# Optimization experiments

Measured on AMD Instinct MI355X. Metric: run time of the kernel, lower is better.

The kernel has to match this reference:

```python
import jax, jax.numpy as jnp
import numpy as np

PI = np.pi
WIN = (8, 8)
N = WIN[0] * WIN[1]          # 64 tokens per window
NUM_HEADS = 8
DIM = 256
HEAD_DIM = DIM // NUM_HEADS  # 32
P = 4                        # Fourier series order (hardcoded in module)
W_RES = 64                   # input_resolution[1]
SCALE = HEAD_DIM ** -0.5
B_ = 1024                    # num_windows * batch


def _azimuth():
    # relative_coords[:, :, 1] from the torch module: relative column offsets
    ch = np.arange(WIN[0])
    cw = np.arange(WIN[1])
    gh, gw = np.meshgrid(ch, cw, indexing='ij')
    cf = np.stack([gh.ravel(), gw.ravel()])          # (2, N)
    rel = cf[:, :, None] - cf[:, None, :]            # (2, N, N)
    return jnp.asarray(rel[1], dtype=jnp.float32)    # (N, N)


def setup_inputs() -> dict:
    key = jax.random.key(0)
    ks = jax.random.split(key, 12)
    std = 0.02
    return {
        'x': jax.random.normal(ks[0], (B_, N, DIM), dtype=jnp.float32),
        'D': jax.random.uniform(ks[1], (B_, N), dtype=jnp.float32),
        'a_p': std * jax.random.normal(ks[2], (P + 1, NUM_HEADS), dtype=jnp.float32),
        'b_p': std * jax.random.normal(ks[3], (P, NUM_HEADS), dtype=jnp.float32),
        'a_r': std * jax.random.normal(ks[4], (P + 1, NUM_HEADS), dtype=jnp.float32),
        'b_r': std * jax.random.normal(ks[5], (P, NUM_HEADS), dtype=jnp.float32),
        'qkv_w': std * jax.random.normal(ks[6], (3 * DIM, DIM), dtype=jnp.float32),
        'qkv_b': jnp.zeros((3 * DIM,), dtype=jnp.float32),
        'proj_w': std * jax.random.normal(ks[7], (DIM, DIM), dtype=jnp.float32),
        'proj_b': jnp.zeros((DIM,), dtype=jnp.float32),
    }


def reference(x, D, a_p, b_p, a_r, b_r, qkv_w, qkv_b, proj_w, proj_b):
    B, n, C = x.shape

    # ---- azimuth Fourier bias: A_phi, shape (H, N, N) ----
    az = _azimuth() * (2.0 * PI / W_RES)                       # (N, N)
    ii = jnp.arange(1, P + 1, dtype=x.dtype)[:, None, None]    # (P, 1, 1)
    cosP = jnp.cos(ii * az)                                    # (P, N, N)
    sinP = jnp.sin(ii * az)
    A_phi = (jnp.einsum('ph,pij->hij', a_p[1:], cosP)
             + jnp.einsum('ph,pij->hij', b_p, sinP)) / P + a_p[0][:, None, None]

    # ---- radius Fourier bias: A_r, shape (B, N, N, H); rad[b,i,j] = D[b,j] - D[b,i] ----
    rad = D[:, None, :] - D[:, :, None]                        # (B, N, N)
    r_max = 2.0                                                # module overwrites r_max = 2
    A_r = jnp.zeros(rad.shape + (NUM_HEADS,), dtype=x.dtype)
    for i in range(1, P + 1):
        arg = rad * (2.0 * PI * i / r_max)
        A_r = A_r + jnp.cos(arg)[..., None] * a_r[i] + jnp.sin(arg)[..., None] * b_r[i - 1]
    A_r = A_r / P + a_r[0]                                     # (B, N, N, H)

    # ---- attention ----
    qkv = (x @ qkv_w.T + qkv_b).reshape(B, n, 3, NUM_HEADS, HEAD_DIM)
    qkv = qkv.transpose(2, 0, 3, 1, 4)                         # (3, B, H, N, hd)
    q, k, v = qkv[0], qkv[1], qkv[2]
    attn = jnp.einsum('bhid,bhjd->bhij', q * SCALE, k)
    attn = attn + A_phi[None] + A_r.transpose(0, 3, 1, 2)
    attn = jax.nn.softmax(attn, axis=-1)
    out = jnp.einsum('bhij,bhjd->bhid', attn, v)
    out = out.transpose(0, 2, 1, 3).reshape(B, n, C)
    return out @ proj_w.T + proj_b
```

## Files before the change

kernel.cpp:

```cpp
#include <hip/hip_runtime.h>
#include <hip/hip_bf16.h>


using short8  = __attribute__((ext_vector_type(8))) short;
using floatx4 = __attribute__((ext_vector_type(4))) float;

#define PI_F    3.14159265358979323846f
#define SCALE_F 0.17677669529663687f

__global__ void prep_kernel(const float* __restrict__ qw,
                            const float* __restrict__ pw,
                            __hip_bfloat16* __restrict__ dst) {
  int g = blockIdx.x * 256 + threadIdx.x;
  const float4* src;
  __hip_bfloat16* d;
  if (g < 49152) { src = (const float4*)qw + g; d = dst + g * 4; }
  else { int g2 = g - 49152; src = (const float4*)pw + g2; d = dst + 196608 + g2 * 4; }
  float4 v = *src;
  d[0] = __float2bfloat16(v.x);
  d[1] = __float2bfloat16(v.y);
  d[2] = __float2bfloat16(v.z);
  d[3] = __float2bfloat16(v.w);
}

__device__ __forceinline__ void fourier_feats(float dv, int col, float* f) {
  float s1, c1; __sincosf(PI_F * dv, &s1, &c1);
  float c2 = c1*c1 - s1*s1, s2 = 2.f*s1*c1;
  float c3 = c2*c1 - s2*s1, s3 = s2*c1 + c2*s1;
  float c4 = c2*c2 - s2*s2, s4 = 2.f*s2*c2;
  float sa1, ca1; __sincosf((2.f * PI_F / 64.f) * (float)col, &sa1, &ca1);
  float ca2 = ca1*ca1 - sa1*sa1, sa2 = 2.f*sa1*ca1;
  float ca3 = ca2*ca1 - sa2*sa1, sa3 = sa2*ca1 + ca2*sa1;
  float ca4 = ca2*ca2 - sa2*sa2, sa4 = 2.f*sa2*ca2;
  f[0]=c1;  f[1]=c2;  f[2]=c3;  f[3]=c4;
  f[4]=s1;  f[5]=s2;  f[6]=s3;  f[7]=s4;
  f[8]=ca1; f[9]=ca2; f[10]=ca3; f[11]=ca4;
  f[12]=sa1; f[13]=sa2; f[14]=sa3; f[15]=sa4;
}

__global__ __launch_bounds__(512, 2) void fused_kernel(
    const float* __restrict__ x, const float* __restrict__ D,
    const float* __restrict__ a_p, const float* __restrict__ b_p,
    const float* __restrict__ a_r, const float* __restrict__ b_r,
    const __hip_bfloat16* __restrict__ wq, const float* __restrict__ qkv_b,
    const __hip_bfloat16* __restrict__ pwb, const float* __restrict__ pb,
    float* __restrict__ out)
{
  constexpr int LDX = 264, LDQ = 264, LDK = 264, LDQf = 40, LDKm = 136,
                LDVt = 72, LDP = 72, LDO = 264;
  __shared__ __align__(16) __hip_bfloat16 sScr[64 * 264];
  __shared__ __align__(16) __hip_bfloat16 sQ  [64 * 264];
  __shared__ __align__(16) __hip_bfloat16 sK  [64 * 264];
  __shared__ __align__(16) __hip_bfloat16 sQf [64 * 40];
  __shared__ __align__(16) __hip_bfloat16 sKm [64 * 136];
  __shared__ __align__(16) __hip_bfloat16 sVt [256 * 72];

  const int tid = threadIdx.x;
  const int lane = tid & 63, w = tid >> 6;
  const int laneN = lane & 15, laneQ = lane >> 4;
  const int b = blockIdx.x;
  const floatx4 fzero = {0.f, 0.f, 0.f, 0.f};
  const short8 zero8 = {0, 0, 0, 0, 0, 0, 0, 0};

  const float4* xg = (const float4*)(x + (size_t)b * 16384);
  #pragma unroll
  for (int it = 0; it < 8; ++it) {
    int g = tid + it * 512;
    float4 v = xg[g];
    int t = g >> 6, c = (g & 63) * 4;
    __hip_bfloat16* p = &sScr[t * LDX + c];
    p[0] = __float2bfloat16(v.x); p[1] = __float2bfloat16(v.y);
    p[2] = __float2bfloat16(v.z); p[3] = __float2bfloat16(v.w);
  }
  if (tid < 64) {
    float f[16];
    fourier_feats(D[b * 64 + tid], tid & 7, f);
    #pragma unroll
    for (int i = 0; i < 16; ++i) sQf[tid * LDQf + i] = __float2bfloat16(f[i]);
    #pragma unroll
    for (int i = 16; i < 32; ++i) sQf[tid * LDQf + i] = __float2bfloat16(0.f);
  }
  __syncthreads();

  {
    int t = tid >> 3, hh = tid & 7;
    float f[16];
    fourier_feats(D[b * 64 + t], t & 7, f);
    #pragma unroll
    for (int p = 0; p < 4; ++p) {
      float ar = a_r[(p + 1) * 8 + hh], br = b_r[p * 8 + hh];
      float ap = a_p[(p + 1) * 8 + hh], bp = b_p[p * 8 + hh];
      float cr = f[p], sr = f[4 + p], ca = f[8 + p], sa = f[12 + p];
      sKm[t * LDKm + hh * 16 +  0 + p] = __float2bfloat16((ar * cr + br * sr) * 0.25f);
      sKm[t * LDKm + hh * 16 +  4 + p] = __float2bfloat16((ar * sr - br * cr) * 0.25f);
      sKm[t * LDKm + hh * 16 +  8 + p] = __float2bfloat16((ap * ca - bp * sa) * 0.25f);
      sKm[t * LDKm + hh * 16 + 12 + p] = __float2bfloat16((ap * sa + bp * ca) * 0.25f);
    }
  }

  short8 afq[4][8];
  #pragma unroll
  for (int mt = 0; mt < 4; ++mt)
    #pragma unroll
    for (int kk = 0; kk < 8; ++kk)
      afq[mt][kk] = *(const short8*)&sScr[(mt * 16 + laneN) * LDX + kk * 32 + laneQ * 8];

  #pragma unroll
  for (int ni = 0; ni < 6; ++ni) {
    int col0 = (w * 6 + ni) * 16;
    float bias = qkv_b[col0 + laneN];
    short8 bq[8];
    #pragma unroll
    for (int kk = 0; kk < 8; ++kk)
      bq[kk] = *(const short8*)&wq[(size_t)(col0 + laneN) * 256 + kk * 32 + laneQ * 8];
    floatx4 acc[4] = {fzero, fzero, fzero, fzero};
    #pragma unroll
    for (int kk = 0; kk < 8; ++kk)
      #pragma unroll
      for (int mt = 0; mt < 4; ++mt)
        acc[mt] = __builtin_amdgcn_mfma_f32_16x16x32_bf16(afq[mt][kk], bq[kk], acc[mt], 0, 0, 0);
    if (col0 < 256) {
      #pragma unroll
      for (int mt = 0; mt < 4; ++mt)
        #pragma unroll
        for (int r = 0; r < 4; ++r)
          sQ[(mt * 16 + laneQ * 4 + r) * LDQ + col0 + laneN] =
              __float2bfloat16((acc[mt][r] + bias) * SCALE_F);
    } else if (col0 < 512) {
      #pragma unroll
      for (int mt = 0; mt < 4; ++mt)
        #pragma unroll
        for (int r = 0; r < 4; ++r)
          sK[(mt * 16 + laneQ * 4 + r) * LDK + (col0 - 256) + laneN] =
              __float2bfloat16(acc[mt][r] + bias);
    } else {
      int vd = col0 - 512 + laneN;
      #pragma unroll
      for (int mt = 0; mt < 4; ++mt)
        #pragma unroll
        for (int r = 0; r < 4; ++r)
          sVt[vd * LDVt + (mt * 16 + laneQ * 4 + r)] = __float2bfloat16(acc[mt][r] + bias);
    }
  }
  __syncthreads();

  const int h = w;
  short8 qf0[4], qf1[4], kf0[4], kf1[4];
  #pragma unroll
  for (int mt = 0; mt < 4; ++mt) {
    qf0[mt] = *(const short8*)&sQ[(mt * 16 + laneN) * LDQ + h * 32 + laneQ * 8];
    qf1[mt] = *(const short8*)&sQf[(mt * 16 + laneN) * LDQf + laneQ * 8];
  }
  #pragma unroll
  for (int nt = 0; nt < 4; ++nt) {
    kf0[nt] = *(const short8*)&sK[(nt * 16 + laneN) * LDK + h * 32 + laneQ * 8];
    short8 km = *(const short8*)&sKm[(nt * 16 + laneN) * LDKm + h * 16 + (laneQ & 1) * 8];
    kf1[nt] = (laneQ < 2) ? km : zero8;
  }
  floatx4 s[4][4];
  #pragma unroll
  for (int mt = 0; mt < 4; ++mt)
    #pragma unroll
    for (int nt = 0; nt < 4; ++nt) {
      s[mt][nt] = __builtin_amdgcn_mfma_f32_16x16x32_bf16(qf0[mt], kf0[nt], fzero, 0, 0, 0);
      s[mt][nt] = __builtin_amdgcn_mfma_f32_16x16x32_bf16(qf1[mt], kf1[nt], s[mt][nt], 0, 0, 0);
    }

  short8 vb[2][2];
  #pragma unroll
  for (int ont = 0; ont < 2; ++ont)
    #pragma unroll
    for (int kk = 0; kk < 2; ++kk)
      vb[ont][kk] = *(const short8*)&sVt[(h * 32 + ont * 16 + laneN) * LDVt + kk * 32 + laneQ * 8];

  floatx4 oacc[4][2];
  __hip_bfloat16* Pw = &sScr[w * 16 * LDP];
  #pragma unroll
  for (int mt = 0; mt < 4; ++mt) {
    #pragma unroll
    for (int r = 0; r < 4; ++r) {
      float mx = fmaxf(fmaxf(s[mt][0][r], s[mt][1][r]), fmaxf(s[mt][2][r], s[mt][3][r]));
      mx = fmaxf(mx, __shfl_xor(mx, 1));
      mx = fmaxf(mx, __shfl_xor(mx, 2));
      mx = fmaxf(mx, __shfl_xor(mx, 4));
      mx = fmaxf(mx, __shfl_xor(mx, 8));
      float e0 = __expf(s[mt][0][r] - mx), e1 = __expf(s[mt][1][r] - mx);
      float e2 = __expf(s[mt][2][r] - mx), e3 = __expf(s[mt][3][r] - mx);
      float sum = e0 + e1 + e2 + e3;
      sum += __shfl_xor(sum, 1);
      sum += __shfl_xor(sum, 2);
      sum += __shfl_xor(sum, 4);
      sum += __shfl_xor(sum, 8);
      float inv = __builtin_amdgcn_rcpf(sum);
      int pr = laneQ * 4 + r;
      Pw[pr * LDP +  0 + laneN] = __float2bfloat16(e0 * inv);
      Pw[pr * LDP + 16 + laneN] = __float2bfloat16(e1 * inv);
      Pw[pr * LDP + 32 + laneN] = __float2bfloat16(e2 * inv);
      Pw[pr * LDP + 48 + laneN] = __float2bfloat16(e3 * inv);
    }
    short8 pf0 = *(const short8*)&Pw[laneN * LDP + laneQ * 8];
    short8 pf1 = *(const short8*)&Pw[laneN * LDP + 32 + laneQ * 8];
    #pragma unroll
    for (int ont = 0; ont < 2; ++ont) {
      oacc[mt][ont] = __builtin_amdgcn_mfma_f32_16x16x32_bf16(pf0, vb[ont][0], fzero, 0, 0, 0);
      oacc[mt][ont] = __builtin_amdgcn_mfma_f32_16x16x32_bf16(pf1, vb[ont][1], oacc[mt][ont], 0, 0, 0);
    }
  }
  __syncthreads();

  #pragma unroll
  for (int mt = 0; mt < 4; ++mt)
    #pragma unroll
    for (int ont = 0; ont < 2; ++ont)
      #pragma unroll
      for (int r = 0; r < 4; ++r)
        sScr[(mt * 16 + laneQ * 4 + r) * LDO + h * 32 + ont * 16 + laneN] =
            __float2bfloat16(oacc[mt][ont][r]);
  __syncthreads();

  const int col0 = w * 32;
  floatx4 pacc[4][2];
  #pragma unroll
  for (int mt = 0; mt < 4; ++mt) { pacc[mt][0] = fzero; pacc[mt][1] = fzero; }
  #pragma unroll
  for (int kk = 0; kk < 8; ++kk) {
    short8 pa[4], pbf[2];
    #pragma unroll
    for (int mt = 0; mt < 4; ++mt)
      pa[mt] = *(const short8*)&sScr[(mt * 16 + laneN) * LDO + kk * 32 + laneQ * 8];
    #pragma unroll
    for (int n2 = 0; n2 < 2; ++n2)
      pbf[n2] = *(const short8*)&pwb[(size_t)(col0 + n2 * 16 + laneN) * 256 + kk * 32 + laneQ * 8];
    #pragma unroll
    for (int mt = 0; mt < 4; ++mt)
      #pragma unroll
      for (int n2 = 0; n2 < 2; ++n2)
        pacc[mt][n2] = __builtin_amdgcn_mfma_f32_16x16x32_bf16(pa[mt], pbf[n2], pacc[mt][n2], 0, 0, 0);
  }
  float bias0 = pb[col0 + laneN], bias1 = pb[col0 + 16 + laneN];
  float* og = out + (size_t)b * 16384;
  #pragma unroll
  for (int mt = 0; mt < 4; ++mt)
    #pragma unroll
    for (int n2 = 0; n2 < 2; ++n2)
      #pragma unroll
      for (int r = 0; r < 4; ++r)
        og[(mt * 16 + laneQ * 4 + r) * 256 + col0 + n2 * 16 + laneN] =
            pacc[mt][n2][r] + (n2 ? bias1 : bias0);
}

extern "C" void kernel_launch(void* const* d_in, const int* in_sizes, int n_in,
                              void* d_out, int out_size, void* d_ws, size_t ws_size,
                              hipStream_t stream) {
  const float* x      = (const float*)d_in[0];
  const float* D      = (const float*)d_in[1];
  const float* a_p    = (const float*)d_in[2];
  const float* b_p    = (const float*)d_in[3];
  const float* a_r    = (const float*)d_in[4];
  const float* b_r    = (const float*)d_in[5];
  const float* qkv_w  = (const float*)d_in[6];
  const float* qkv_b  = (const float*)d_in[7];
  const float* proj_w = (const float*)d_in[8];
  const float* proj_b = (const float*)d_in[9];

  __hip_bfloat16* wq  = (__hip_bfloat16*)d_ws;
  __hip_bfloat16* pwb = wq + 196608;
  float* out = (float*)d_out;

  prep_kernel<<<256, 256, 0, stream>>>(qkv_w, proj_w, wq);
  fused_kernel<<<1024, 512, 0, stream>>>(x, D, a_p, b_p, a_r, b_r, wq, qkv_b,
                                         pwb, proj_b, out);
}
```

Measured before the change: 211.0 us.

## Double block to 1024 threads and split work across 16 waves with vectorized LDS stores

Launches 16 waves per window instead of 8. Each wave computes a 16-column slice of Q, K and V, half a head's query rows in attention, and a 16-column slice of the projection. MFMA operands are swapped so that results come out transposed and can be written as packed 4- or 8-element vector stores to LDS and as float4 global stores, instead of scalar bf16 and fp32 stores. The goal is more latency hiding per window and fewer LDS and global store instructions, at the cost of more per-wave K/V fragment loads and higher register pressure under launch bounds of 1024 threads with 4 blocks.

```diff
diff --git a/kernel.cpp b/kernel.cpp
--- a/kernel.cpp
+++ b/kernel.cpp
@@ -3,10 +3,16 @@
 
 
 using short8  = __attribute__((ext_vector_type(8))) short;
+using short4v = __attribute__((ext_vector_type(4))) short;
 using floatx4 = __attribute__((ext_vector_type(4))) float;
 
 #define PI_F    3.14159265358979323846f
 #define SCALE_F 0.17677669529663687f
+
+__device__ __forceinline__ short bfs(float x) {
+  __hip_bfloat16 h = __float2bfloat16(x);
+  return __builtin_bit_cast(short, h);
+}
 
 __global__ void prep_kernel(const float* __restrict__ qw,
                             const float* __restrict__ pw,
@@ -38,7 +44,7 @@
   f[12]=sa1; f[13]=sa2; f[14]=sa3; f[15]=sa4;
 }
 
-__global__ __launch_bounds__(512, 2) void fused_kernel(
+__global__ __launch_bounds__(1024, 4) void fused_kernel(
     const float* __restrict__ x, const float* __restrict__ D,
     const float* __restrict__ a_p, const float* __restrict__ b_p,
     const float* __restrict__ a_r, const float* __restrict__ b_r,
@@ -47,8 +53,8 @@
     float* __restrict__ out)
 {
   constexpr int LDX = 264, LDQ = 264, LDK = 264, LDQf = 40, LDKm = 136,
-                LDVt = 72, LDP = 72, LDO = 264;
-  __shared__ __align__(16) __hip_bfloat16 sScr[64 * 264];
+                LDVt = 72, LDP = 68, LDO = 264;
+  __shared__ __align__(16) __hip_bfloat16 sScr[17408];
   __shared__ __align__(16) __hip_bfloat16 sQ  [64 * 264];
   __shared__ __align__(16) __hip_bfloat16 sK  [64 * 264];
   __shared__ __align__(16) __hip_bfloat16 sQf [64 * 40];
@@ -64,108 +70,96 @@
 
   const float4* xg = (const float4*)(x + (size_t)b * 16384);
   #pragma unroll
-  for (int it = 0; it < 8; ++it) {
-    int g = tid + it * 512;
+  for (int it = 0; it < 4; ++it) {
+    int g = tid + it * 1024;
     float4 v = xg[g];
     int t = g >> 6, c = (g & 63) * 4;
-    __hip_bfloat16* p = &sScr[t * LDX + c];
-    p[0] = __float2bfloat16(v.x); p[1] = __float2bfloat16(v.y);
-    p[2] = __float2bfloat16(v.z); p[3] = __float2bfloat16(v.w);
+    short4v pk = { bfs(v.x), bfs(v.y), bfs(v.z), bfs(v.w) };
+    *(short4v*)&sScr[t * LDX + c] = pk;
   }
   if (tid < 64) {
     float f[16];
     fourier_feats(D[b * 64 + tid], tid & 7, f);
-    #pragma unroll
-    for (int i = 0; i < 16; ++i) sQf[tid * LDQf + i] = __float2bfloat16(f[i]);
-    #pragma unroll
-    for (int i = 16; i < 32; ++i) sQf[tid * LDQf + i] = __float2bfloat16(0.f);
-  }
-  __syncthreads();
-
-  {
+    short8 q0, q1;
+    #pragma unroll
+    for (int i = 0; i < 8; ++i) { q0[i] = bfs(f[i]); q1[i] = bfs(f[8 + i]); }
+    *(short8*)&sQf[tid * LDQf +  0] = q0;
+    *(short8*)&sQf[tid * LDQf +  8] = q1;
+    *(short8*)&sQf[tid * LDQf + 16] = zero8;
+    *(short8*)&sQf[tid * LDQf + 24] = zero8;
+  }
+  if (tid < 512) {
     int t = tid >> 3, hh = tid & 7;
     float f[16];
     fourier_feats(D[b * 64 + t], t & 7, f);
+    short8 v0, v1;
     #pragma unroll
     for (int p = 0; p < 4; ++p) {
       float ar = a_r[(p + 1) * 8 + hh], br = b_r[p * 8 + hh];
       float ap = a_p[(p + 1) * 8 + hh], bp = b_p[p * 8 + hh];
       float cr = f[p], sr = f[4 + p], ca = f[8 + p], sa = f[12 + p];
-      sKm[t * LDKm + hh * 16 +  0 + p] = __float2bfloat16((ar * cr + br * sr) * 0.25f);
-      sKm[t * LDKm + hh * 16 +  4 + p] = __float2bfloat16((ar * sr - br * cr) * 0.25f);
-      sKm[t * LDKm + hh * 16 +  8 + p] = __float2bfloat16((ap * ca - bp * sa) * 0.25f);
-      sKm[t * LDKm + hh * 16 + 12 + p] = __float2bfloat16((ap * sa + bp * ca) * 0.25f);
-    }
-  }
-
-  short8 afq[4][8];
-  #pragma unroll
-  for (int mt = 0; mt < 4; ++mt)
-    #pragma unroll
-    for (int kk = 0; kk < 8; ++kk)
-      afq[mt][kk] = *(const short8*)&sScr[(mt * 16 + laneN) * LDX + kk * 32 + laneQ * 8];
-
-  #pragma unroll
-  for (int ni = 0; ni < 6; ++ni) {
-    int col0 = (w * 6 + ni) * 16;
-    float bias = qkv_b[col0 + laneN];
-    short8 bq[8];
-    #pragma unroll
-    for (int kk = 0; kk < 8; ++kk)
-      bq[kk] = *(const short8*)&wq[(size_t)(col0 + laneN) * 256 + kk * 32 + laneQ * 8];
-    floatx4 acc[4] = {fzero, fzero, fzero, fzero};
-    #pragma unroll
-    for (int kk = 0; kk < 8; ++kk)
+      v0[p]     = bfs((ar * cr + br * sr) * 0.25f);
+      v0[4 + p] = bfs((ar * sr - br * cr) * 0.25f);
+      v1[p]     = bfs((ap * ca - bp * sa) * 0.25f);
+      v1[4 + p] = bfs((ap * sa + bp * ca) * 0.25f);
+    }
+    *(short8*)&sKm[t * LDKm + hh * 16 + 0] = v0;
+    *(short8*)&sKm[t * LDKm + hh * 16 + 8] = v1;
+  }
+  __syncthreads();
+
+  {
+    const __hip_bfloat16* w0 = wq + (size_t)(      w * 16 + laneN) * 256;
+    const __hip_bfloat16* w1 = wq + (size_t)(256 + w * 16 + laneN) * 256;
+    const __hip_bfloat16* w2 = wq + (size_t)(512 + w * 16 + laneN) * 256;
+    floatx4 accQ[4], accK[4], accV[4];
+    #pragma unroll
+    for (int mt = 0; mt < 4; ++mt) { accQ[mt] = fzero; accK[mt] = fzero; accV[mt] = fzero; }
+    #pragma unroll
+    for (int kk = 0; kk < 8; ++kk) {
+      short8 a4[4];
       #pragma unroll
       for (int mt = 0; mt < 4; ++mt)
-        acc[mt] = __builtin_amdgcn_mfma_f32_16x16x32_bf16(afq[mt][kk], bq[kk], acc[mt], 0, 0, 0);
-    if (col0 < 256) {
-      #pragma unroll
-      for (int mt = 0; mt < 4; ++mt)
-        #pragma unroll
-        for (int r = 0; r < 4; ++r)
-          sQ[(mt * 16 + laneQ * 4 + r) * LDQ + col0 + laneN] =
-              __float2bfloat16((acc[mt][r] + bias) * SCALE_F);
-    } else if (col0 < 512) {
-      #pragma unroll
-      for (int mt = 0; mt < 4; ++mt)
-        #pragma unroll
-        for (int r = 0; r < 4; ++r)
-          sK[(mt * 16 + laneQ * 4 + r) * LDK + (col0 - 256) + laneN] =
-              __float2bfloat16(acc[mt][r] + bias);
-    } else {
-      int vd = col0 - 512 + laneN;
-      #pragma unroll
-      for (int mt = 0; mt < 4; ++mt)
-        #pragma unroll
-        for (int r = 0; r < 4; ++r)
-          sVt[vd * LDVt + (mt * 16 + laneQ * 4 + r)] = __float2bfloat16(acc[mt][r] + bias);
-    }
-  }
-  __syncthreads();
-
-  const int h = w;
-  short8 qf0[4], qf1[4], kf0[4], kf1[4];
-  #pragma unroll
-  for (int mt = 0; mt < 4; ++mt) {
-    qf0[mt] = *(const short8*)&sQ[(mt * 16 + laneN) * LDQ + h * 32 + laneQ * 8];
-    qf1[mt] = *(const short8*)&sQf[(mt * 16 + laneN) * LDQf + laneQ * 8];
-  }
+        a4[mt] = *(const short8*)&sScr[(mt * 16 + laneN) * LDX + kk * 32 + laneQ * 8];
+      short8 b0 = *(const short8*)&w0[kk * 32 + laneQ * 8];
+      short8 b1 = *(const short8*)&w1[kk * 32 + laneQ * 8];
+      short8 b2 = *(const short8*)&w2[kk * 32 + laneQ * 8];
+      #pragma unroll
+      for (int mt = 0; mt < 4; ++mt) {
+        accQ[mt] = __builtin_amdgcn_mfma_f32_16x16x32_bf16(b0, a4[mt], accQ[mt], 0, 0, 0);
+        accK[mt] = __builtin_amdgcn_mfma_f32_16x16x32_bf16(b1, a4[mt], accK[mt], 0, 0, 0);
+        accV[mt] = __builtin_amdgcn_mfma_f32_16x16x32_bf16(a4[mt], b2, accV[mt], 0, 0, 0);
+      }
+    }
+    float4 bq4 = *(const float4*)&qkv_b[      w * 16 + laneQ * 4];
+    float4 bk4 = *(const float4*)&qkv_b[256 + w * 16 + laneQ * 4];
+    float bv   = qkv_b[512 + w * 16 + laneN];
+    float bqa[4] = {bq4.x, bq4.y, bq4.z, bq4.w};
+    float bka[4] = {bk4.x, bk4.y, bk4.z, bk4.w};
+    #pragma unroll
+    for (int mt = 0; mt < 4; ++mt) {
+      short4v pq, pk, pv;
+      #pragma unroll
+      for (int r = 0; r < 4; ++r) {
+        pq[r] = bfs((accQ[mt][r] + bqa[r]) * SCALE_F);
+        pk[r] = bfs(accK[mt][r] + bka[r]);
+        pv[r] = bfs(accV[mt][r] + bv);
+      }
+      *(short4v*)&sQ [(mt * 16 + laneN) * LDQ + w * 16 + laneQ * 4] = pq;
+      *(short4v*)&sK [(mt * 16 + laneN) * LDK + w * 16 + laneQ * 4] = pk;
+      *(short4v*)&sVt[(w * 16 + laneN) * LDVt + mt * 16 + laneQ * 4] = pv;
+    }
+  }
+  __syncthreads();
+
+  const int h = w >> 1, gm0 = (w & 1) * 2;
+  short8 kf0[4], kf1[4];
   #pragma unroll
   for (int nt = 0; nt < 4; ++nt) {
     kf0[nt] = *(const short8*)&sK[(nt * 16 + laneN) * LDK + h * 32 + laneQ * 8];
     short8 km = *(const short8*)&sKm[(nt * 16 + laneN) * LDKm + h * 16 + (laneQ & 1) * 8];
     kf1[nt] = (laneQ < 2) ? km : zero8;
   }
-  floatx4 s[4][4];
-  #pragma unroll
-  for (int mt = 0; mt < 4; ++mt)
-    #pragma unroll
-    for (int nt = 0; nt < 4; ++nt) {
-      s[mt][nt] = __builtin_amdgcn_mfma_f32_16x16x32_bf16(qf0[mt], kf0[nt], fzero, 0, 0, 0);
-      s[mt][nt] = __builtin_amdgcn_mfma_f32_16x16x32_bf16(qf1[mt], kf1[nt], s[mt][nt], 0, 0, 0);
-    }
-
   short8 vb[2][2];
   #pragma unroll
   for (int ont = 0; ont < 2; ++ont)
@@ -173,19 +167,28 @@
     for (int kk = 0; kk < 2; ++kk)
       vb[ont][kk] = *(const short8*)&sVt[(h * 32 + ont * 16 + laneN) * LDVt + kk * 32 + laneQ * 8];
 
-  floatx4 oacc[4][2];
+  floatx4 oacc[2][2];
   __hip_bfloat16* Pw = &sScr[w * 16 * LDP];
   #pragma unroll
-  for (int mt = 0; mt < 4; ++mt) {
+  for (int m = 0; m < 2; ++m) {
+    const int gm = gm0 + m;
+    short8 q0 = *(const short8*)&sQ [(gm * 16 + laneN) * LDQ + h * 32 + laneQ * 8];
+    short8 q1 = *(const short8*)&sQf[(gm * 16 + laneN) * LDQf + laneQ * 8];
+    floatx4 s[4];
+    #pragma unroll
+    for (int nt = 0; nt < 4; ++nt) {
+      s[nt] = __builtin_amdgcn_mfma_f32_16x16x32_bf16(q0, kf0[nt], fzero, 0, 0, 0);
+      s[nt] = __builtin_amdgcn_mfma_f32_16x16x32_bf16(q1, kf1[nt], s[nt], 0, 0, 0);
+    }
     #pragma unroll
     for (int r = 0; r < 4; ++r) {
-      float mx = fmaxf(fmaxf(s[mt][0][r], s[mt][1][r]), fmaxf(s[mt][2][r], s[mt][3][r]));
+      float mx = fmaxf(fmaxf(s[0][r], s[1][r]), fmaxf(s[2][r], s[3][r]));
       mx = fmaxf(mx, __shfl_xor(mx, 1));
       mx = fmaxf(mx, __shfl_xor(mx, 2));
       mx = fmaxf(mx, __shfl_xor(mx, 4));
       mx = fmaxf(mx, __shfl_xor(mx, 8));
-      float e0 = __expf(s[mt][0][r] - mx), e1 = __expf(s[mt][1][r] - mx);
-      float e2 = __expf(s[mt][2][r] - mx), e3 = __expf(s[mt][3][r] - mx);
+      float e0 = __expf(s[0][r] - mx), e1 = __expf(s[1][r] - mx);
+      float e2 = __expf(s[2][r] - mx), e3 = __expf(s[3][r] - mx);
       float sum = e0 + e1 + e2 + e3;
       sum += __shfl_xor(sum, 1);
       sum += __shfl_xor(sum, 2);
@@ -198,55 +201,54 @@
       Pw[pr * LDP + 32 + laneN] = __float2bfloat16(e2 * inv);
       Pw[pr * LDP + 48 + laneN] = __float2bfloat16(e3 * inv);
     }
-    short8 pf0 = *(const short8*)&Pw[laneN * LDP + laneQ * 8];
-    short8 pf1 = *(const short8*)&Pw[laneN * LDP + 32 + laneQ * 8];
+    short4v p0a = *(const short4v*)&Pw[laneN * LDP + laneQ * 8];
+    short4v p0b = *(const short4v*)&Pw[laneN * LDP + laneQ * 8 + 4];
+    short4v p1a = *(const short4v*)&Pw[laneN * LDP + 32 + laneQ * 8];
+    short4v p1b = *(const short4v*)&Pw[laneN * LDP + 36 + laneQ * 8];
+    short8 pf0 = __builtin_shufflevector(p0a, p0b, 0, 1, 2, 3, 4, 5, 6, 7);
+    short8 pf1 = __builtin_shufflevector(p1a, p1b, 0, 1, 2, 3, 4, 5, 6, 7);
     #pragma unroll
     for (int ont = 0; ont < 2; ++ont) {
-      oacc[mt][ont] = __builtin_amdgcn_mfma_f32_16x16x32_bf16(pf0, vb[ont][0], fzero, 0, 0, 0);
-      oacc[mt][ont] = __builtin_amdgcn_mfma_f32_16x16x32_bf16(pf1, vb[ont][1], oacc[mt][ont], 0, 0, 0);
-    }
-  }
-  __syncthreads();
-
-  #pragma unroll
-  for (int mt = 0; mt < 4; ++mt)
-    #pragma unroll
-    for (int ont = 0; ont < 2; ++ont)
-      #pragma unroll
-      for (int r = 0; r < 4; ++r)
-        sScr[(mt * 16 + laneQ * 4 + r) * LDO + h * 32 + ont * 16 + laneN] =
-            __float2bfloat16(oacc[mt][ont][r]);
-  __syncthreads();
-
-  const int col0 = w * 32;
-  floatx4 pacc[4][2];
-  #pragma unroll
-  for (int mt = 0; mt < 4; ++mt) { pacc[mt][0] = fzero; pacc[mt][1] = fzero; }
+      oacc[m][ont] = __builtin_amdgcn_mfma_f32_16x16x32_bf16(vb[ont][0], pf0, fzero, 0, 0, 0);
+      oacc[m][ont] = __builtin_amdgcn_mfma_f32_16x16x32_bf16(vb[ont][1], pf1, oacc[m][ont], 0, 0, 0);
+    }
+  }
+  __syncthreads();
+
+  #pragma unroll
+  for (int m = 0; m < 2; ++m)
+    #pragma unroll
+    for (int ont = 0; ont < 2; ++ont) {
+      short4v pk;
+      #pragma unroll
+      for (int r = 0; r < 4; ++r) pk[r] = bfs(oacc[m][ont][r]);
+      *(short4v*)&sScr[((gm0 + m) * 16 + laneN) * LDO + h * 32 + ont * 16 + laneQ * 4] = pk;
+    }
+  __syncthreads();
+
+  const int col0 = w * 16;
+  floatx4 pacc[4] = {fzero, fzero, fzero, fzero};
+  const __hip_bfloat16* prow = pwb + (size_t)(col0 + laneN) * 256;
   #pragma unroll
   for (int kk = 0; kk < 8; ++kk) {
-    short8 pa[4], pbf[2];
-    #pragma unroll
-    for (int mt = 0; mt < 4; ++mt)
-      pa[mt] = *(const short8*)&sScr[(mt * 16 + laneN) * LDO + kk * 32 + laneQ * 8];
-    #pragma unroll
-    for (int n2 = 0; n2 < 2; ++n2)
-      pbf[n2] = *(const short8*)&pwb[(size_t)(col0 + n2 * 16 + laneN) * 256 + kk * 32 + laneQ * 8];
-    #pragma unroll
-    for (int mt = 0; mt < 4; ++mt)
-      #pragma unroll
-      for (int n2 = 0; n2 < 2; ++n2)
-        pacc[mt][n2] = __builtin_amdgcn_mfma_f32_16x16x32_bf16(pa[mt], pbf[n2], pacc[mt][n2], 0, 0, 0);
-  }
-  float bias0 = pb[col0 + laneN], bias1 = pb[col0 + 16 + laneN];
+    short8 pbf = *(const short8*)&prow[kk * 32 + laneQ * 8];
+    #pragma unroll
+    for (int mt = 0; mt < 4; ++mt) {
+      short8 pa = *(const short8*)&sScr[(mt * 16 + laneN) * LDO + kk * 32 + laneQ * 8];
+      pacc[mt] = __builtin_amdgcn_mfma_f32_16x16x32_bf16(pbf, pa, pacc[mt], 0, 0, 0);
+    }
+  }
+  float4 bias4 = *(const float4*)&pb[col0 + laneQ * 4];
   float* og = out + (size_t)b * 16384;
   #pragma unroll
-  for (int mt = 0; mt < 4; ++mt)
-    #pragma unroll
-    for (int n2 = 0; n2 < 2; ++n2)
-      #pragma unroll
-      for (int r = 0; r < 4; ++r)
-        og[(mt * 16 + laneQ * 4 + r) * 256 + col0 + n2 * 16 + laneN] =
-            pacc[mt][n2][r] + (n2 ? bias1 : bias0);
+  for (int mt = 0; mt < 4; ++mt) {
+    float4 o4;
+    o4.x = pacc[mt][0] + bias4.x;
+    o4.y = pacc[mt][1] + bias4.y;
+    o4.z = pacc[mt][2] + bias4.z;
+    o4.w = pacc[mt][3] + bias4.w;
+    *(float4*)&og[(mt * 16 + laneN) * 256 + col0 + laneQ * 4] = o4;
+  }
 }
 
 extern "C" void kernel_launch(void* const* d_in, const int* in_sizes, int n_in,
@@ -268,6 +270,6 @@
   float* out = (float*)d_out;
 
   prep_kernel<<<256, 256, 0, stream>>>(qkv_w, proj_w, wq);
-  fused_kernel<<<1024, 512, 0, stream>>>(x, D, a_p, b_p, a_r, b_r, wq, qkv_b,
-                                         pwb, proj_b, out);
-}
+  fused_kernel<<<1024, 1024, 0, stream>>>(x, D, a_p, b_p, a_r, b_r, wq, qkv_b,
+                                          pwb, proj_b, out);
+}
```

After: 215.2 us. About the same (+2.0%).
